# Optimization experiments

Measured on AMD Instinct MI355X. Metric: run time of the kernel, lower is better.

## Reference

```python
import jax, jax.numpy as jnp
import numpy as np
import itertools

DIM = 384; KEY_DIM = 32; NH = 8; RES = 7; N = RES * RES
D = 4 * KEY_DIM; DH = D * NH; NHKD = KEY_DIM * NH; HID = 4 * DIM
B = 512
SCALE = KEY_DIM ** -0.5

def ste_round(x):
    return x + jax.lax.stop_gradient(jnp.round(x) - x)

def ste_floor(x):
    return x + jax.lax.stop_gradient(jnp.floor(x) - x)

def quant_act(x, bits=8):
    # dynamic per-tensor symmetric fake-quant (QuantAct)
    qmax = 2.0 ** (bits - 1) - 1
    s = jnp.maximum(jnp.max(jnp.abs(x)) / qmax, 1e-8)
    return jnp.clip(ste_round(x / s), -qmax, qmax) * s, s

def quant_w(w, bits=8):
    # per-output-channel symmetric weight fake-quant
    qmax = 2.0 ** (bits - 1) - 1
    red = tuple(range(1, w.ndim))
    s = jnp.maximum(jnp.max(jnp.abs(w), axis=red, keepdims=True) / qmax, 1e-8)
    return jnp.clip(ste_round(w / s), -qmax, qmax) * s

def conv(x, w, b, stride=1, pad=0, groups=1):
    # QuantBNConv2d with BN folded into (w, b)
    y = jax.lax.conv_general_dilated(
        x, quant_w(w), (stride, stride), [(pad, pad), (pad, pad)],
        dimension_numbers=('NCHW', 'OIHW', 'NCHW'), feature_group_count=groups)
    return y + b[None, :, None, None]

def head_mix(attn, w, b):
    # talking-heads 1x1 QuantConv2d over the head axis
    return jnp.einsum('oi,bixy->boxy', quant_w(w)[:, :, 0, 0], attn) + b[None, :, None, None]

def int_softmax(x, sf, out_bit=16):
    # I-BERT style integer softmax (2nd-order poly approx of exp) over last axis
    n = 30
    c0 = 0.35815147
    x_int = x / sf
    x_int = x_int - jnp.max(x_int, axis=-1, keepdims=True)
    x0_int = jnp.floor(-0.6931 / sf)  # ln(2) in integer domain
    x_int = jnp.maximum(x_int, n * x0_int)
    q = ste_floor(x_int / x0_int)
    r = x_int - x0_int * q
    b_int = jnp.floor((0.96963238 / c0) / sf)
    c_int = jnp.floor((1.0 / c0) / (sf * sf))
    z = (r + b_int) * r + c_int
    exp_int = jnp.clip(ste_floor(z * jnp.exp2(n - q)), 0.0, None)
    exp, exp_sf = quant_act(exp_int * (c0 * sf * sf / 2.0 ** n), 16)
    exp_int = exp / exp_sf
    factor = ste_floor(2.0 ** 32 / jnp.sum(exp_int, axis=-1, keepdims=True))
    exp_int = ste_floor(exp_int * factor / 2.0 ** (32 - out_bit))
    sf_out = 1.0 / 2.0 ** out_bit
    return exp_int * sf_out, sf_out

def _forward(x, act_sf, wq, bq, wk, bk, wv, bv, wvl, bvl, attn_biases,
             wth1, bth1, wth2, bth2, wproj, bproj,
             wfc1, bfc1, wmid, bmid, wfc2, bfc2, ls1, ls2, bias_idxs):
    Bn = x.shape[0]
    # --- token mixer (Q_Attention4D, stride=None) ---
    q, _ = quant_act(conv(x, wq, bq))
    q = q.reshape(Bn, NH, KEY_DIM, N).transpose(0, 1, 3, 2)   # (B,H,N,kd)
    k, _ = quant_act(conv(x, wk, bk))
    k = k.reshape(Bn, NH, KEY_DIM, N)                          # (B,H,kd,N)
    vf, _ = quant_act(conv(x, wv, bv))
    vl, _ = quant_act(conv(vf, wvl, bvl, pad=1, groups=DH))    # depthwise 3x3 local branch
    v = vf.reshape(Bn, NH, D, N).transpose(0, 1, 3, 2)         # (B,H,N,d)
    attn = jnp.einsum('bhnk,bhkm->bhnm', q, k) * SCALE
    attn = attn + attn_biases[:, bias_idxs]                    # (H,N,N) relative position bias
    attn, _ = quant_act(attn, 8)                               # quant_pre_th1
    attn = head_mix(attn, wth1, bth1)                          # talking_head1
    attn, a_sf = quant_act(attn, 8)                            # quant_attn
    attn, a_sf = int_softmax(attn, a_sf, 16)
    attn = head_mix(attn, wth2, bth2)                          # talking_head2
    attn, _ = quant_act(attn, 8)                               # quant_postsm
    out = jnp.einsum('bhnm,bhmd->bhnd', attn, v)
    out = out.transpose(0, 1, 3, 2).reshape(Bn, DH, RES, RES) + vl
    out, _ = quant_act(out)                                    # quant_av_res
    out = jax.nn.relu(out)                                     # proj_act
    out, _ = quant_act(out)                                    # proj_in_quant
    out = conv(out, wproj, bproj)
    out, _ = quant_act(out)                                    # proj_quant
    x1, _ = quant_act(x + ls1[None] * out)                     # residual 1 + quant_res1
    # --- Q_Mlp (mid_conv=True, ReLU) ---
    h = jax.nn.relu(conv(x1, wfc1, bfc1))
    h, _ = quant_act(h)
    h = jax.nn.relu(conv(h, wmid, bmid, pad=1, groups=HID))
    h, _ = quant_act(h)
    h = conv(h, wfc2, bfc2)
    h, _ = quant_act(h)
    out2, out_sf = quant_act(x1 + ls2[None] * h)               # residual 2 + quant_res2
    return out2, out_sf

def setup_inputs():
    key = jax.random.key(0)
    ks = jax.random.split(key, 16)
    rn = lambda k, shp: (0.02 * jax.random.normal(k, shp)).astype(jnp.float32)
    z = lambda n: jnp.zeros((n,), jnp.float32)
    # rebuild attention_bias_idxs exactly as in __init__
    pts = list(itertools.product(range(RES), range(RES)))
    offs, idxs = {}, []
    for p1 in pts:
        for p2 in pts:
            o = (abs(p1[0] - p2[0]), abs(p1[1] - p2[1]))
            if o not in offs:
                offs[o] = len(offs)
            idxs.append(offs[o])
    bias_idxs = jnp.asarray(np.array(idxs, dtype=np.int32).reshape(N, N))
    return dict(
        x=jax.random.normal(ks[0], (B, DIM, RES, RES), jnp.float32),
        act_sf=jnp.ones((1,), jnp.float32),
        wq=rn(ks[1], (NHKD, DIM, 1, 1)), bq=z(NHKD),
        wk=rn(ks[2], (NHKD, DIM, 1, 1)), bk=z(NHKD),
        wv=rn(ks[3], (DH, DIM, 1, 1)), bv=z(DH),
        wvl=rn(ks[4], (DH, 1, 3, 3)), bvl=z(DH),
        attn_biases=rn(ks[5], (NH, len(offs))),
        wth1=rn(ks[6], (NH, NH, 1, 1)), bth1=z(NH),
        wth2=rn(ks[7], (NH, NH, 1, 1)), bth2=z(NH),
        wproj=rn(ks[8], (DIM, DH, 1, 1)), bproj=z(DIM),
        wfc1=rn(ks[9], (HID, DIM, 1, 1)), bfc1=z(HID),
        wmid=rn(ks[10], (HID, 1, 3, 3)), bmid=z(HID),
        wfc2=rn(ks[11], (DIM, HID, 1, 1)), bfc2=z(DIM),
        ls1=1e-5 * jnp.ones((DIM, 1, 1), jnp.float32),
        ls2=1e-5 * jnp.ones((DIM, 1, 1), jnp.float32),
        bias_idxs=bias_idxs)

def reference(x, act_sf, wq, bq, wk, bk, wv, bv, wvl, bvl, attn_biases,
              wth1, bth1, wth2, bth2, wproj, bproj,
              wfc1, bfc1, wmid, bmid, wfc2, bfc2, ls1, ls2, bias_idxs):
    return _forward(x, act_sf, wq, bq, wk, bk, wv, bv, wvl, bvl, attn_biases,
                    wth1, bth1, wth2, bth2, wproj, bproj,
                    wfc1, bfc1, wmid, bmid, wfc2, bfc2, ls1, ls2, bias_idxs)
```

## Files before the change

### kernel.cpp

```cpp
#include <hip/hip_runtime.h>

typedef unsigned short u16;
typedef unsigned int u32;
typedef float f32x4 __attribute__((ext_vector_type(4)));
typedef short bf16x8 __attribute__((ext_vector_type(8)));
typedef short s16x4 __attribute__((ext_vector_type(4)));


__device__ __forceinline__ u16 f2bf(float f){
  u32 x = __float_as_uint(f);
  x += 0x7fffu + ((x >> 16) & 1u);
  return (u16)(x >> 16);
}
__device__ __forceinline__ float bf2f(u16 u){ return __uint_as_float(((u32)u) << 16); }
__device__ __forceinline__ float qsc(float m, float qmax){ return fmaxf(m / qmax, 1e-8f); }
__device__ __forceinline__ float fq(float x, float s){
  return fminf(fmaxf(rintf(x / s), -127.f), 127.f) * s;
}
__device__ __forceinline__ float fqi(float x, float s, float inv){
  return fminf(fmaxf(rintf(x * inv), -127.f), 127.f) * s;
}
__device__ __forceinline__ float rdmx(const float* mx, int reg){
  float m = mx[reg];
  #pragma unroll
  for (int s = 1; s < 16; ++s) m = fmaxf(m, mx[s*64 + reg]);
  return m;
}
__device__ __forceinline__ void blockMaxTo(float* mx, int reg, float v){
  __shared__ float red[8];
  #pragma unroll
  for (int o = 32; o > 0; o >>= 1) v = fmaxf(v, __shfl_xor(v, o, 64));
  const int wid = threadIdx.x >> 6;
  const int nw = (int)(blockDim.x + 63) >> 6;
  __syncthreads();
  if ((threadIdx.x & 63) == 0) red[wid] = v;
  __syncthreads();
  if (threadIdx.x == 0){
    float m = red[0];
    for (int i = 1; i < nw; ++i) m = fmaxf(m, red[i]);
    const int slot = (blockIdx.x + blockIdx.y*4) & 15;
    atomicMax((int*)&mx[slot*64 + reg], __float_as_int(m));
  }
}
__device__ __forceinline__ void blockMax2To(float* mx, int r0i, float v0, int r1i, float v1){
  __shared__ float r0[8], r1[8];
  #pragma unroll
  for (int o = 32; o > 0; o >>= 1){
    v0 = fmaxf(v0, __shfl_xor(v0, o, 64));
    v1 = fmaxf(v1, __shfl_xor(v1, o, 64));
  }
  const int wid = threadIdx.x >> 6;
  const int nw = (int)(blockDim.x + 63) >> 6;
  __syncthreads();
  if ((threadIdx.x & 63) == 0){ r0[wid] = v0; r1[wid] = v1; }
  __syncthreads();
  if (threadIdx.x == 0){
    float m0 = r0[0], m1 = r1[0];
    for (int i = 1; i < nw; ++i){ m0 = fmaxf(m0, r0[i]); m1 = fmaxf(m1, r1[i]); }
    const int slot = (blockIdx.x + blockIdx.y*4) & 15;
    atomicMax((int*)&mx[slot*64 + r0i], __float_as_int(m0));
    atomicMax((int*)&mx[slot*64 + r1i], __float_as_int(m1));
  }
}

__device__ __forceinline__ void gload16(const void* g, void* l){
  __builtin_amdgcn_global_load_lds((const __attribute__((address_space(1))) u32*)g,
                                   (__attribute__((address_space(3))) u32*)l, 16, 0, 0);
}

__global__ void zeromx(float* mx){
  for (int j = threadIdx.x; j < 1024; j += 256) mx[j] = 0.f;
}

__global__ __launch_bounds__(128) void wquant(
    const float* wq, const float* wk, const float* wv, const float* wproj,
    const float* wfc1, const float* wfc2, const float* wvl, const float* wmid,
    const float* wth1, const float* wth2,
    const float* bq, const float* bk, const float* bv,
    const float* ab, const int* idxs,
    u16* wqkv_b, u16* wproj_b, u16* wfc1_b, u16* wfc2_b,
    float* wvl_q, float* wmid_q, float* wth1_q, float* wth2_q, float* biasqkv,
    float* biasx)
{
  const int tid = threadIdx.x;
  const int bid = blockIdx.x;
  if (bid == 6416){
    for (int j = tid; j < 1536; j += 128){
      float v = (j < 256) ? bq[j] : ((j < 512) ? bk[j - 256] : bv[j - 512]);
      biasqkv[j] = v;
    }
    return;
  }
  if (bid >= 6417){
    const int h = bid - 6417;
    for (int j = tid; j < 2401; j += 128)
      biasx[h*2401 + j] = ab[h*49 + idxs[j]];
    return;
  }
  const int rows[10] = {256,256,1024,384,1536,384,1024,1536,8,8};
  int seg = 0, r = bid;
  while (r >= rows[seg]) { r -= rows[seg]; ++seg; }
  int len = 0;
  const float* src = nullptr; u16* db = nullptr; float* df = nullptr;
  switch (seg){
    case 0: len = 384;  src = wq    + r*384;  db = wqkv_b + r*384;        break;
    case 1: len = 384;  src = wk    + r*384;  db = wqkv_b + (256+r)*384;  break;
    case 2: len = 384;  src = wv    + r*384;  db = wqkv_b + (512+r)*384;  break;
    case 3: len = 1024; src = wproj + r*1024; db = wproj_b + r*1024;      break;
    case 4: len = 384;  src = wfc1  + r*384;  db = wfc1_b + r*384;        break;
    case 5: len = 1536; src = wfc2  + r*1536; db = wfc2_b + r*1536;       break;
    case 6: len = 9;    src = wvl   + r*9;    df = wvl_q + r*9;           break;
    case 7: len = 9;    src = wmid  + r*9;    df = wmid_q + r*9;          break;
    case 8: len = 8;    src = wth1  + r*8;    df = wth1_q + r*8;          break;
    default: len = 8;   src = wth2  + r*8;    df = wth2_q + r*8;          break;
  }
  float lm = 0.f;
  for (int j = tid; j < len; j += 128) lm = fmaxf(lm, fabsf(src[j]));
  __shared__ float red[128];
  red[tid] = lm; __syncthreads();
  for (int s = 64; s > 0; s >>= 1){
    if (tid < s) red[tid] = fmaxf(red[tid], red[tid + s]);
    __syncthreads();
  }
  float s = fmaxf(red[0] / 127.f, 1e-8f);
  for (int j = tid; j < len; j += 128){
    float v = fminf(fmaxf(rintf(src[j] / s), -127.f), 127.f) * s;
    if (db) db[j] = f2bf(v); else df[j] = v;
  }
}

__global__ __launch_bounds__(256) void xpose(const float* __restrict__ x, u16* __restrict__ xT){
  const int b = blockIdx.x;
  __shared__ u16 xb[18816];
  const int tid = threadIdx.x;
  for (int jj = tid; jj < 4704; jj += 256){
    const float4 v = *(const float4*)&x[(size_t)b*18816 + jj*4];
    xb[jj*4+0] = f2bf(v.x); xb[jj*4+1] = f2bf(v.y);
    xb[jj*4+2] = f2bf(v.z); xb[jj*4+3] = f2bf(v.w);
  }
  __syncthreads();
  for (int jj = tid; jj < 4704; jj += 256){
    int j = jj*4, p = j / 384, c = j - p*384;
    s16x4 o;
    #pragma unroll
    for (int u = 0; u < 4; ++u) o[u] = (short)xb[(c+u)*49 + p];
    *(s16x4*)&xT[(size_t)b*18816 + j] = o;
  }
}

__global__ __launch_bounds__(256) void gemm_bt(
    const u16* __restrict__ A, const u16* __restrict__ Bt,
    const float* __restrict__ bias, u16* __restrict__ C,
    float* __restrict__ mx, int N, int K, int epi, int region, int aquant)
{
  const int nx = gridDim.x;
  const int nwg = nx * gridDim.y;
  const int orig = blockIdx.x + nx * blockIdx.y;
  const int q8 = nwg >> 3, r8 = nwg & 7;
  const int xcd = orig & 7;
  const int lid = ((xcd < r8) ? xcd*(q8+1) : r8*(q8+1) + (xcd - r8)*q8) + (orig >> 3);
  const int n0 = (lid % nx) * 128;
  const int m0 = (lid / nx) * 128;
  __shared__ __align__(16) u16 As[128*64];
  __shared__ __align__(16) u16 Bs[128*64];
  const int tid = threadIdx.x;
  const int lane = tid & 63, wid = tid >> 6;
  const int wr = wid >> 1, wc = wid & 1;
  float qa_s0 = 1.f, qa_i0 = 1.f, qa_s1 = 1.f, qa_i1 = 1.f;
  if (aquant == 1){
    qa_s0 = qsc(rdmx(mx,7), 127.f); qa_i0 = 1.f/qa_s0;
    float posq = fq(rdmx(mx,8), qa_s0);
    qa_s1 = fmaxf(posq / 127.f, 1e-8f); qa_i1 = 1.f/qa_s1;
  } else if (aquant == 2){
    qa_s0 = qsc(rdmx(mx,12), 127.f); qa_i0 = 1.f/qa_s0;
  }
  f32x4 acc[4][4] = {};
  const int nsteps = K >> 6;
  for (int s = 0; s < nsteps; ++s){
    const int k0 = s << 6;
    #pragma unroll
    for (int j = 0; j < 4; ++j){
      int boff = j*4096 + tid*16;
      int row = boff >> 7;
      int ce  = (((boff & 127) ^ ((row & 7) << 4)) >> 1);
      if (aquant == 0){
        gload16(A + (size_t)(m0 + row)*K + k0 + ce, (char*)As + boff);
      } else {
        uint4 va = *(const uint4*)(A + (size_t)(m0 + row)*K + k0 + ce);
        u16* e = (u16*)&va;
        #pragma unroll
        for (int u = 0; u < 8; ++u){
          float f = bf2f(e[u]);
          if (aquant == 1){
            f = fmaxf(fqi(f, qa_s0, qa_i0), 0.f);
            f = fqi(f, qa_s1, qa_i1);
          } else {
            f = fqi(f, qa_s0, qa_i0);
          }
          e[u] = f2bf(f);
        }
        *(uint4*)((char*)As + boff) = va;
      }
      gload16(Bt + (size_t)(n0 + row)*K + k0 + ce, (char*)Bs + boff);
    }
    __syncthreads();
    #pragma unroll
    for (int kk = 0; kk < 2; ++kk){
      bf16x8 af[4], bfr[4];
      #pragma unroll
      for (int i = 0; i < 4; ++i){
        int ar = wr*64 + i*16 + (lane & 15);
        int aidx = (ar*64 + kk*32 + (lane >> 4)*8) ^ ((ar & 7) << 3);
        af[i]  = *(const bf16x8*)&As[aidx];
        int br = wc*64 + i*16 + (lane & 15);
        int bidx = (br*64 + kk*32 + (lane >> 4)*8) ^ ((br & 7) << 3);
        bfr[i] = *(const bf16x8*)&Bs[bidx];
      }
      #pragma unroll
      for (int i = 0; i < 4; ++i){
        #pragma unroll
        for (int j = 0; j < 4; ++j){
          acc[i][j] = __builtin_amdgcn_mfma_f32_16x16x32_bf16(af[i], bfr[j], acc[i][j], 0, 0, 0);
        }
      }
    }
    __syncthreads();
  }
  float lm = 0.f;
  #pragma unroll
  for (int i = 0; i < 4; ++i){
    int rbase = m0 + wr*64 + i*16 + ((lane >> 4) << 2);
    #pragma unroll
    for (int j = 0; j < 4; ++j){
      int col = n0 + wc*64 + j*16 + (lane & 15);
      float bv = bias[col];
      #pragma unroll
      for (int q = 0; q < 4; ++q){
        float v = acc[i][j][q] + bv;
        if (epi == 2) v = fmaxf(v, 0.f);
        C[(size_t)(rbase + q)*N + col] = f2bf(v);
        lm = fmaxf(lm, (epi == 2) ? v : fabsf(v));
      }
    }
  }
  int reg = region;
  if (epi == 1) reg = (n0 < 256) ? 0 : ((n0 < 512) ? 1 : 2);
  blockMaxTo(mx, reg, lm);
}

__global__ __launch_bounds__(256) void attn_qk(
    const u16* __restrict__ qkv, const float* __restrict__ biasx,
    const float* __restrict__ wv9, const float* __restrict__ bvl,
    u16* __restrict__ S, u16* __restrict__ vlb, float* __restrict__ mx)
{
  const int h = blockIdx.x;
  __shared__ __align__(16) float xin[6272];
  __shared__ __align__(16) u16 Qb[64*40];
  __shared__ __align__(16) u16 Kb[64*40];
  const float sq = qsc(rdmx(mx,0), 127.f), sk = qsc(rdmx(mx,1), 127.f), sv = qsc(rdmx(mx,2), 127.f);
  const float iq = 1.f/sq, ik = 1.f/sk, iv = 1.f/sv;
  const int tid = threadIdx.x;
  const int lane = tid & 63, wid = tid >> 6;
  const int c = tid & 127, half = tid >> 7;
  float w9[9];
  #pragma unroll
  for (int t = 0; t < 9; ++t) w9[t] = wv9[h*1152 + c*9 + t];
  const float bb = bvl[h*128 + c];
  const float sscale = (sq * sk) * 0.17677669529663687f;
  const float* bx = biasx + h*2401;
  const int col = wid*16 + (lane & 15);
  float lm = 0.f, lmV = 0.f;
  for (int bb4 = 0; bb4 < 4; ++bb4){
    const int b = blockIdx.y*4 + bb4;
    __syncthreads();
    for (int j = tid; j < 196; j += 256){
      int n = j >> 2, d0 = (j & 3)*8;
      size_t base = (size_t)(b*49 + n)*1536;
      const bf16x8 qv = *(const bf16x8*)&qkv[base + h*32 + d0];
      const bf16x8 kv = *(const bf16x8*)&qkv[base + 256 + h*32 + d0];
      bf16x8 qo, ko;
      #pragma unroll
      for (int u = 0; u < 8; ++u){
        qo[u] = (short)f2bf(fminf(fmaxf(rintf(bf2f((u16)qv[u]) * iq), -127.f), 127.f));
        ko[u] = (short)f2bf(fminf(fmaxf(rintf(bf2f((u16)kv[u]) * ik), -127.f), 127.f));
      }
      *(bf16x8*)&Qb[n*40 + d0] = qo;
      *(bf16x8*)&Kb[n*40 + d0] = ko;
    }
    for (int j = tid; j < 784; j += 256){
      int p = j >> 4, dg = j & 15;
      const bf16x8 vv = *(const bf16x8*)&qkv[(size_t)(b*49 + p)*1536 + 512 + h*128 + dg*8];
      #pragma unroll
      for (int u = 0; u < 8; ++u)
        xin[p*128 + dg*8 + u] = fqi(bf2f((u16)vv[u]), sv, iv);
    }
    __syncthreads();
    {
      const int p0 = half*25, p1 = half ? 49 : 25;
      for (int p = p0; p < p1; ++p){
        const int py = p / 7, px = p - py*7;
        float acc = bb;
        #pragma unroll
        for (int dy = 0; dy < 3; ++dy){
          const int yy = py + dy - 1;
          if (yy < 0 || yy > 6) continue;
          #pragma unroll
          for (int dx = 0; dx < 3; ++dx){
            const int xx = px + dx - 1;
            if (xx < 0 || xx > 6) continue;
            acc += xin[(yy*7 + xx)*128 + c] * w9[dy*3 + dx];
          }
        }
        lmV = fmaxf(lmV, fabsf(acc));
        vlb[(size_t)(b*49 + p)*1024 + h*128 + c] = f2bf(acc);
      }
    }
    f32x4 acc[4] = {};
    {
      const bf16x8 bfr = *(const bf16x8*)&Kb[(wid*16 + (lane & 15))*40 + (lane >> 4)*8];
      #pragma unroll
      for (int i = 0; i < 4; ++i){
        const bf16x8 af = *(const bf16x8*)&Qb[(i*16 + (lane & 15))*40 + (lane >> 4)*8];
        acc[i] = __builtin_amdgcn_mfma_f32_16x16x32_bf16(af, bfr, acc[i], 0, 0, 0);
      }
    }
    if (col < 49){
      const size_t so = ((size_t)b*8 + h)*2401;
      #pragma unroll
      for (int i = 0; i < 4; ++i){
        #pragma unroll
        for (int q = 0; q < 4; ++q){
          const int row = i*16 + ((lane >> 4) << 2) + q;
          if (row < 49){
            float v = acc[i][q] * sscale + bx[row*49 + col];
            S[so + row*49 + col] = f2bf(v);
            lm = fmaxf(lm, fabsf(v));
          }
        }
      }
    }
  }
  blockMax2To(mx, 4, lm, 3, lmV);
}

__global__ __launch_bounds__(256) void th1k(
    const u16* S, const float* w1, const float* b1, u16* T, float* mx)
{
  const int b = blockIdx.y;
  const int j = blockIdx.x*256 + threadIdx.x;
  __shared__ float wsh[64];
  __shared__ float bsh[8];
  if (threadIdx.x < 64) wsh[threadIdx.x] = w1[threadIdx.x];
  if (threadIdx.x < 8)  bsh[threadIdx.x] = b1[threadIdx.x];
  __syncthreads();
  float lm = 0.f;
  if (j < 2401){
    const float s1 = qsc(rdmx(mx,4), 127.f);
    const float i1 = 1.f/s1;
    float a[8];
    #pragma unroll
    for (int h = 0; h < 8; ++h) a[h] = fqi(bf2f(S[((size_t)b*8 + h)*2401 + j]), s1, i1);
    float o8[8];
    #pragma unroll
    for (int o = 0; o < 8; ++o){
      float t = bsh[o];
      #pragma unroll
      for (int h = 0; h < 8; ++h) t += wsh[o*8 + h] * a[h];
      o8[o] = t;
      lm = fmaxf(lm, fabsf(t));
    }
    #pragma unroll
    for (int o = 0; o < 8; ++o) T[((size_t)b*8 + o)*2401 + j] = f2bf(o8[o]);
  }
  blockMaxTo(mx, 5, lm);
}

__global__ __launch_bounds__(256) void smth2(
    const u16* T, const float* w2, const float* b2, u16* U, float* mx)
{
  const int b = blockIdx.x;
  __shared__ u16 P[19208];
  __shared__ float wsh[64];
  __shared__ float bsh[8];
  const float sa = qsc(rdmx(mx,5), 127.f), ia = 1.f/sa;
  const int tid = threadIdx.x;
  if (tid < 64) wsh[tid] = w2[tid];
  if (tid < 8)  bsh[tid] = b2[tid];
  for (int j = tid; j < 19208; j += 256){
    float k = fminf(fmaxf(rintf(bf2f(T[(size_t)b*19208 + j]) * ia), -127.f), 127.f);
    P[j] = f2bf(k);
  }
  __syncthreads();
  const float x0 = floorf(-0.6931f / sa);
  const float ix0 = 1.f / x0;
  const float bi = floorf((0.96963238f / 0.35815147f) / sa);
  const float ci = floorf((1.0f / 0.35815147f) / (sa * sa));
  const float Kc = ((0.35815147f * sa) * sa) * (1.f/1073741824.f);
  const float maxv = (ci * 1073741824.f) * Kc;
  const float se = fmaxf(maxv / 32767.f, 1e-8f);
  const float ise = 1.f / se;
  const float clampLo = 30.f * x0;
  for (int r = tid; r < 392; r += 256){
    u16* pr = &P[r*49];
    float rmax = -1e30f;
    for (int m = 0; m < 49; ++m) rmax = fmaxf(rmax, bf2f(pr[m]));
    float rsum = 0.f;
    for (int m = 0; m < 49; ++m){
      float xi = bf2f(pr[m]) - rmax;
      xi = fmaxf(xi, clampLo);
      float qd = floorf(xi * ix0);
      float rr = xi - x0*qd;
      float z = (rr + bi)*rr + ci;
      float ei = fmaxf(floorf(z * exp2f(30.f - qd)), 0.f);
      float e2 = fminf(fmaxf(rintf((ei * Kc) * ise), -32767.f), 32767.f);
      u16 eb = f2bf(e2);
      pr[m] = eb;
      rsum += bf2f(eb);
    }
    const float factor = floorf(4294967296.f / rsum);
    for (int m = 0; m < 49; ++m){
      float p = floorf((bf2f(pr[m]) * factor) * (1.f/65536.f)) * (1.f/65536.f);
      pr[m] = f2bf(p);
    }
  }
  __syncthreads();
  float lm = 0.f;
  for (int j = tid; j < 19208; j += 256){
    int o = j / 2401, rem = j - o*2401;
    float t = bsh[o];
    #pragma unroll
    for (int h = 0; h < 8; ++h) t += wsh[o*8 + h] * bf2f(P[h*2401 + rem]);
    U[(size_t)b*19208 + j] = f2bf(t);
    lm = fmaxf(lm, fabsf(t));
  }
  blockMaxTo(mx, 6, lm);
}

__global__ __launch_bounds__(256) void attn_v(
    const u16* __restrict__ qkv, const u16* __restrict__ U,
    u16* __restrict__ av, float* __restrict__ mx)
{
  const int h = blockIdx.x, b = blockIdx.y;
  __shared__ __align__(16) u16 Pb[64*68];
  __shared__ __align__(16) u16 Vt[128*66];
  const float s3 = qsc(rdmx(mx,6), 127.f), sv = qsc(rdmx(mx,2), 127.f), svl = qsc(rdmx(mx,3), 127.f);
  const float i3 = 1.f/s3, iv = 1.f/sv, il = 1.f/svl;
  const float s3sv = s3 * sv;
  const int tid = threadIdx.x;
  const int lane = tid & 63, wid = tid >> 6;
  const int col0 = wid * 32;
  const int ca = col0 + (lane & 15), cb = ca + 16;
  u16 vlrA[16], vlrB[16];
  {
    const size_t vbase = (size_t)(b*49)*1024 + h*128;
    #pragma unroll
    for (int i = 0; i < 4; ++i){
      #pragma unroll
      for (int q = 0; q < 4; ++q){
        const int row = i*16 + ((lane >> 4) << 2) + q;
        const int rr = (row < 49) ? row : 48;
        vlrA[i*4+q] = av[vbase + (size_t)rr*1024 + ca];
        vlrB[i*4+q] = av[vbase + (size_t)rr*1024 + cb];
      }
    }
  }
  for (int j = tid; j < 64*19; j += 256){ int n = j/19, m = 49 + (j - n*19); Pb[n*68 + m] = 0; }
  for (int j = tid; j < 128*17; j += 256){ int d = j/17, m = 49 + (j - d*17); Vt[d*66 + m] = 0; }
  for (int j = tid; j < 2401; j += 256){
    int n = j / 49, m = j - n*49;
    float k = fminf(fmaxf(rintf(bf2f(U[((size_t)b*8 + h)*2401 + j]) * i3), -127.f), 127.f);
    Pb[n*68 + m] = f2bf(k);
  }
  {
    const int dp = lane * 2, mc = wid;
    const int mend = (mc == 3) ? 49 : (mc*13 + 13);
    const size_t base = (size_t)(b*49)*1536 + 512 + h*128 + dp;
    for (int m = mc*13; m < mend; ++m){
      u32 two = *(const u32*)&qkv[base + (size_t)m*1536];
      float k0 = fminf(fmaxf(rintf(bf2f((u16)(two & 0xffffu)) * iv), -127.f), 127.f);
      float k1 = fminf(fmaxf(rintf(bf2f((u16)(two >> 16)) * iv), -127.f), 127.f);
      Vt[dp*66 + m]       = f2bf(k0);
      Vt[(dp + 1)*66 + m] = f2bf(k1);
    }
  }
  __syncthreads();
  f32x4 acc[4][2] = {};
  #pragma unroll
  for (int kk = 0; kk < 2; ++kk){
    bf16x8 af[4], bfr[2];
    #pragma unroll
    for (int i = 0; i < 4; ++i)
      af[i] = *(const bf16x8*)&Pb[(i*16 + (lane & 15))*68 + kk*32 + (lane >> 4)*8];
    #pragma unroll
    for (int j = 0; j < 2; ++j)
      bfr[j] = *(const bf16x8*)&Vt[(col0 + j*16 + (lane & 15))*66 + kk*32 + (lane >> 4)*8];
    #pragma unroll
    for (int i = 0; i < 4; ++i)
      #pragma unroll
      for (int j = 0; j < 2; ++j)
        acc[i][j] = __builtin_amdgcn_mfma_f32_16x16x32_bf16(af[i], bfr[j], acc[i][j], 0, 0, 0);
  }
  float lm = 0.f, lmp = 0.f;
  #pragma unroll
  for (int i = 0; i < 4; ++i){
    #pragma unroll
    for (int q = 0; q < 4; ++q){
      const int row = i*16 + ((lane >> 4) << 2) + q;
      if (row < 49){
        const size_t base = (size_t)(b*49 + row)*1024 + h*128;
        const float vlA = fqi(bf2f(vlrA[i*4+q]), svl, il);
        const float vlB = fqi(bf2f(vlrB[i*4+q]), svl, il);
        const float vA = acc[i][0][q] * s3sv + vlA;
        const float vB = acc[i][1][q] * s3sv + vlB;
        av[base + ca] = f2bf(vA);
        av[base + cb] = f2bf(vB);
        lm = fmaxf(lm, fmaxf(fabsf(vA), fabsf(vB)));
        lmp = fmaxf(lmp, fmaxf(vA, vB));
      }
    }
  }
  blockMax2To(mx, 7, lm, 8, lmp);
}

__global__ __launch_bounds__(256) void res1max(
    const float* __restrict__ x, const u16* __restrict__ praw,
    const float* __restrict__ ls1, float* __restrict__ y1, float* __restrict__ mx)
{
  const int b = blockIdx.x;
  __shared__ float xs[18816];
  __shared__ float lss[384];
  const float sp = qsc(rdmx(mx,9), 127.f);
  const float ip = 1.f / sp;
  const int tid = threadIdx.x;
  for (int jj = tid; jj < 4704; jj += 256)
    *(float4*)&xs[jj*4] = *(const float4*)&x[(size_t)b*18816 + jj*4];
  for (int j = tid; j < 384; j += 256) lss[j] = ls1[j];
  __syncthreads();
  float lm = 0.f;
  for (int jj = tid; jj < 4704; jj += 256){
    int j = jj*4, p = j / 384, c = j - p*384;
    s16x4 pv = *(const s16x4*)&praw[(size_t)b*18816 + j];
    float4 yv;
    #pragma unroll
    for (int u = 0; u < 4; ++u){
      float y = xs[(c+u)*49 + p] + lss[c+u] * fqi(bf2f((u16)pv[u]), sp, ip);
      ((float*)&yv)[u] = y;
      lm = fmaxf(lm, fabsf(y));
    }
    *(float4*)&y1[(size_t)b*18816 + j] = yv;
  }
  blockMaxTo(mx, 10, lm);
}

__global__ void qx1(const float* __restrict__ y1, float* __restrict__ x1f, u16* __restrict__ x1b,
                    const float* __restrict__ mx){
  const float s = qsc(rdmx(mx,10), 127.f);
  const size_t n4 = (size_t)9633792/4;
  for (size_t i = (size_t)blockIdx.x*blockDim.x + threadIdx.x; i < n4; i += (size_t)gridDim.x*blockDim.x){
    float4 v = *(const float4*)(y1 + i*4);
    float4 o; s16x4 ob;
    #pragma unroll
    for (int u = 0; u < 4; ++u){
      float q = fq(((const float*)&v)[u], s);
      ((float*)&o)[u] = q;
      ob[u] = (short)f2bf(q);
    }
    *(float4*)(x1f + i*4) = o;
    *(s16x4*)(x1b + i*4) = ob;
  }
}

__global__ __launch_bounds__(128) void dw_mid(
    const u16* h1, const float* wm9, const float* bmid, u16* m1, float* mx)
{
  const int cc = blockIdx.x, b = blockIdx.y;
  __shared__ float xin[49*132];
  const float sh = qsc(rdmx(mx,11), 127.f);
  const float ih = 1.f / sh;
  const int tid = threadIdx.x;
  for (int j = tid; j < 784; j += 128){
    int p = j >> 4, dg = j & 15;
    const bf16x8 vv = *(const bf16x8*)&h1[(size_t)(b*49 + p)*1536 + cc*128 + dg*8];
    #pragma unroll
    for (int u = 0; u < 8; ++u)
      xin[p*132 + dg*8 + u] = fqi(bf2f((u16)vv[u]), sh, ih);
  }
  __syncthreads();
  const int c = tid;
  float w9[9];
  #pragma unroll
  for (int i = 0; i < 9; ++i) w9[i] = wm9[(cc*128 + c)*9 + i];
  const float bb = bmid[cc*128 + c];
  float col[49];
  #pragma unroll
  for (int p = 0; p < 49; ++p) col[p] = xin[p*132 + c];
  float lm = 0.f;
  #pragma unroll
  for (int p = 0; p < 49; ++p){
    const int py = p / 7, px = p % 7;
    float acc = bb;
    #pragma unroll
    for (int dy = 0; dy < 3; ++dy){
      const int yy = py + dy - 1;
      if (yy < 0 || yy > 6) continue;
      #pragma unroll
      for (int dx = 0; dx < 3; ++dx){
        const int xx = px + dx - 1;
        if (xx < 0 || xx > 6) continue;
        acc += col[yy*7 + xx] * w9[dy*3 + dx];
      }
    }
    acc = fmaxf(acc, 0.f);
    m1[(size_t)(b*49 + p)*1536 + cc*128 + c] = f2bf(acc);
    lm = fmaxf(lm, acc);
  }
  blockMaxTo(mx, 12, lm);
}

__global__ __launch_bounds__(256) void res2max(
    const float* __restrict__ x1f, const u16* __restrict__ f2,
    const float* __restrict__ ls2, float* __restrict__ y2, float* __restrict__ mx)
{
  const float s = qsc(rdmx(mx,13), 127.f);
  const float is = 1.f / s;
  float lm = 0.f;
  const size_t n4 = (size_t)9633792/4;
  for (size_t i = (size_t)blockIdx.x*blockDim.x + threadIdx.x; i < n4; i += (size_t)gridDim.x*blockDim.x){
    int c0 = (int)((i*4) % 384);
    float4 xv = *(const float4*)(x1f + i*4);
    s16x4 fv = *(const s16x4*)(f2 + i*4);
    float4 yv;
    #pragma unroll
    for (int u = 0; u < 4; ++u){
      float y = ((const float*)&xv)[u] + ls2[c0+u] * fqi(bf2f((u16)fv[u]), s, is);
      ((float*)&yv)[u] = y;
      lm = fmaxf(lm, fabsf(y));
    }
    *(float4*)(y2 + i*4) = yv;
  }
  blockMaxTo(mx, 14, lm);
}

__global__ __launch_bounds__(256) void finalout(
    const float* __restrict__ y2, float* __restrict__ out, const float* __restrict__ mx)
{
  const int b = blockIdx.x;
  __shared__ float os[18816];
  const float s = qsc(rdmx(mx,14), 127.f);
  const int tid = threadIdx.x;
  for (int jj = tid; jj < 4704; jj += 256){
    int j = jj*4, p = j / 384, c = j - p*384;
    float4 yv = *(const float4*)&y2[(size_t)b*18816 + j];
    #pragma unroll
    for (int u = 0; u < 4; ++u)
      os[(c+u)*49 + p] = fq(((const float*)&yv)[u], s);
  }
  __syncthreads();
  for (int jj = tid; jj < 4704; jj += 256)
    *(float4*)&out[(size_t)b*18816 + jj*4] = *(const float4*)&os[jj*4];
  if (b == 0 && tid == 0) out[9633792] = s;
}

extern "C" void kernel_launch(void* const* d_in, const int* in_sizes, int n_in,
                              void* d_out, int out_size, void* d_ws, size_t ws_size,
                              hipStream_t stream)
{
  (void)in_sizes; (void)n_in; (void)out_size; (void)ws_size;
  const float* x    = (const float*)d_in[0];
  const float* wq   = (const float*)d_in[2];
  const float* bq   = (const float*)d_in[3];
  const float* wk   = (const float*)d_in[4];
  const float* bk   = (const float*)d_in[5];
  const float* wv   = (const float*)d_in[6];
  const float* bv   = (const float*)d_in[7];
  const float* wvl  = (const float*)d_in[8];
  const float* bvl  = (const float*)d_in[9];
  const float* ab   = (const float*)d_in[10];
  const float* wth1 = (const float*)d_in[11];
  const float* bth1 = (const float*)d_in[12];
  const float* wth2 = (const float*)d_in[13];
  const float* bth2 = (const float*)d_in[14];
  const float* wproj= (const float*)d_in[15];
  const float* bproj= (const float*)d_in[16];
  const float* wfc1 = (const float*)d_in[17];
  const float* bfc1 = (const float*)d_in[18];
  const float* wmid = (const float*)d_in[19];
  const float* bmid = (const float*)d_in[20];
  const float* wfc2 = (const float*)d_in[21];
  const float* bfc2 = (const float*)d_in[22];
  const float* ls1  = (const float*)d_in[23];
  const float* ls2  = (const float*)d_in[24];
  const int*   idxs = (const int*)d_in[25];
  float* out = (float*)d_out;

  char* w = (char*)d_ws;
  float* biasqkv = (float*)(w + 256);
  u16* wqkv_b    = (u16*)(w + 6400);
  u16* wproj_b   = (u16*)(w + 1186048);
  u16* wfc1_b    = (u16*)(w + 1972480);
  u16* wfc2_b    = (u16*)(w + 3152128);
  float* wvl_q   = (float*)(w + 4331776);
  float* wmid_q  = (float*)(w + 4368640);
  float* wth1_q  = (float*)(w + 4423936);
  float* wth2_q  = (float*)(w + 4424192);
  u16* xT    = (u16*)(w + 4424448);
  u16* praw  = xT;
  u16* x1b   = xT;
  u16* f2raw = xT;
  u16* qkv = (u16*)(w + 23692032);
  u16* h1  = qkv;
  u16* avb = (u16*)(w + 100762368);
  u16* Sb   = (u16*)(w + 152142592);
  float* y1 = (float*)(w + 152142592);
  float* y2 = y1;
  float* biasx = (float*)(w + 190677760);
  float* mx = (float*)(w + 190754816);
  float* x1f = out;

  zeromx<<<1, 256, 0, stream>>>(mx);
  wquant<<<6425, 128, 0, stream>>>(wq, wk, wv, wproj, wfc1, wfc2, wvl, wmid, wth1, wth2,
                                   bq, bk, bv, ab, idxs,
                                   wqkv_b, wproj_b, wfc1_b, wfc2_b,
                                   wvl_q, wmid_q, wth1_q, wth2_q, biasqkv, biasx);
  xpose<<<512, 256, 0, stream>>>(x, xT);
  gemm_bt<<<dim3(12, 196), 256, 0, stream>>>(xT, wqkv_b, biasqkv, qkv, mx, 1536, 384, 1, 0, 0);
  attn_qk<<<dim3(8, 128), 256, 0, stream>>>(qkv, biasx, wvl_q, bvl, Sb, avb, mx);
  th1k<<<dim3(10, 512), 256, 0, stream>>>(Sb, wth1_q, bth1, Sb, mx);
  smth2<<<512, 256, 0, stream>>>(Sb, wth2_q, bth2, Sb, mx);
  attn_v<<<dim3(8, 512), 256, 0, stream>>>(qkv, Sb, avb, mx);
  gemm_bt<<<dim3(3, 196), 256, 0, stream>>>(avb, wproj_b, bproj, praw, mx, 384, 1024, 0, 9, 1);
  res1max<<<512, 256, 0, stream>>>(x, praw, ls1, y1, mx);
  qx1<<<2048, 256, 0, stream>>>(y1, x1f, x1b, mx);
  gemm_bt<<<dim3(12, 196), 256, 0, stream>>>(x1b, wfc1_b, bfc1, h1, mx, 1536, 384, 2, 11, 0);
  dw_mid<<<dim3(12, 512), 128, 0, stream>>>(h1, wmid_q, bmid, h1, mx);
  gemm_bt<<<dim3(3, 196), 256, 0, stream>>>(h1, wfc2_b, bfc2, f2raw, mx, 384, 1536, 0, 13, 2);
  res2max<<<2048, 256, 0, stream>>>(x1f, f2raw, ls2, y2, mx);
  finalout<<<512, 256, 0, stream>>>(y2, out, mx);
}
```

Before: 557.2 us.

## Use 256x128 tiles with XCD-aware block remap for QKV and FC1 GEMMs

Adds a gemm_bt2 kernel that computes a 256x128 output tile per block, reusing each B fragment across two A halves. Block IDs are remapped so consecutive tiles land on the same XCD for better L2 locality. It is used for the QKV and FC1 GEMMs (N=1536, K=384) and halves the grid. The kernel is single-buffered with more accumulator registers, which risks lower occupancy and fewer blocks to spread across CUs.

```diff
diff --git a/kernel.cpp b/kernel.cpp
--- a/kernel.cpp
+++ b/kernel.cpp
@@ -240,6 +240,92 @@
         if (epi == 2) v = fmaxf(v, 0.f);
         C[(size_t)(rbase + q)*N + col] = f2bf(v);
         lm = fmaxf(lm, (epi == 2) ? v : fabsf(v));
+      }
+    }
+  }
+  int reg = region;
+  if (epi == 1) reg = (n0 < 256) ? 0 : ((n0 < 512) ? 1 : 2);
+  blockMaxTo(mx, reg, lm);
+}
+
+__global__ __launch_bounds__(256) void gemm_bt2(
+    const u16* __restrict__ A, const u16* __restrict__ Bt,
+    const float* __restrict__ bias, u16* __restrict__ C,
+    float* __restrict__ mx, int N, int K, int epi, int region)
+{
+  const int nx = gridDim.x;
+  const int nwg = nx * gridDim.y;
+  const int orig = blockIdx.x + nx * blockIdx.y;
+  const int q8 = nwg >> 3, r8 = nwg & 7;
+  const int xcd = orig & 7;
+  const int lid = ((xcd < r8) ? xcd*(q8+1) : r8*(q8+1) + (xcd - r8)*q8) + (orig >> 3);
+  const int n0 = (lid % nx) * 128;
+  const int m0 = (lid / nx) * 256;
+  __shared__ __align__(16) u16 As[2][128*64];
+  __shared__ __align__(16) u16 Bs[128*64];
+  const int tid = threadIdx.x;
+  const int lane = tid & 63, wid = tid >> 6;
+  const int wr = wid >> 1, wc = wid & 1;
+  f32x4 acc[2][4][4] = {};
+  const int nsteps = K >> 6;
+  for (int s = 0; s < nsteps; ++s){
+    const int k0 = s << 6;
+    #pragma unroll
+    for (int j = 0; j < 4; ++j){
+      int boff = j*4096 + tid*16;
+      int row = boff >> 7;
+      int ce  = (((boff & 127) ^ ((row & 7) << 4)) >> 1);
+      gload16(A + (size_t)(m0 + row)*K + k0 + ce,        (char*)As[0] + boff);
+      gload16(A + (size_t)(m0 + 128 + row)*K + k0 + ce,  (char*)As[1] + boff);
+      gload16(Bt + (size_t)(n0 + row)*K + k0 + ce,       (char*)Bs + boff);
+    }
+    __syncthreads();
+    #pragma unroll
+    for (int kk = 0; kk < 2; ++kk){
+      bf16x8 bfr[4];
+      #pragma unroll
+      for (int i = 0; i < 4; ++i){
+        int br = wc*64 + i*16 + (lane & 15);
+        int bidx = (br*64 + kk*32 + (lane >> 4)*8) ^ ((br & 7) << 3);
+        bfr[i] = *(const bf16x8*)&Bs[bidx];
+      }
+      #pragma unroll
+      for (int h = 0; h < 2; ++h){
+        bf16x8 af[4];
+        #pragma unroll
+        for (int i = 0; i < 4; ++i){
+          int ar = wr*64 + i*16 + (lane & 15);
+          int aidx = (ar*64 + kk*32 + (lane >> 4)*8) ^ ((ar & 7) << 3);
+          af[i] = *(const bf16x8*)&As[h][aidx];
+        }
+        #pragma unroll
+        for (int i = 0; i < 4; ++i){
+          #pragma unroll
+          for (int j = 0; j < 4; ++j){
+            acc[h][i][j] = __builtin_amdgcn_mfma_f32_16x16x32_bf16(af[i], bfr[j], acc[h][i][j], 0, 0, 0);
+          }
+        }
+      }
+    }
+    __syncthreads();
+  }
+  float lm = 0.f;
+  #pragma unroll
+  for (int h = 0; h < 2; ++h){
+    #pragma unroll
+    for (int i = 0; i < 4; ++i){
+      int rbase = m0 + h*128 + wr*64 + i*16 + ((lane >> 4) << 2);
+      #pragma unroll
+      for (int j = 0; j < 4; ++j){
+        int col = n0 + wc*64 + j*16 + (lane & 15);
+        float bv = bias[col];
+        #pragma unroll
+        for (int q = 0; q < 4; ++q){
+          float v = acc[h][i][j][q] + bv;
+          if (epi == 2) v = fmaxf(v, 0.f);
+          C[(size_t)(rbase + q)*N + col] = f2bf(v);
+          lm = fmaxf(lm, (epi == 2) ? v : fabsf(v));
+        }
       }
     }
   }
@@ -723,7 +809,7 @@
                                    wqkv_b, wproj_b, wfc1_b, wfc2_b,
                                    wvl_q, wmid_q, wth1_q, wth2_q, biasqkv, biasx);
   xpose<<<512, 256, 0, stream>>>(x, xT);
-  gemm_bt<<<dim3(12, 196), 256, 0, stream>>>(xT, wqkv_b, biasqkv, qkv, mx, 1536, 384, 1, 0, 0);
+  gemm_bt2<<<dim3(12, 98), 256, 0, stream>>>(xT, wqkv_b, biasqkv, qkv, mx, 1536, 384, 1, 0);
   attn_qk<<<dim3(8, 128), 256, 0, stream>>>(qkv, biasx, wvl_q, bvl, Sb, avb, mx);
   th1k<<<dim3(10, 512), 256, 0, stream>>>(Sb, wth1_q, bth1, Sb, mx);
   smth2<<<512, 256, 0, stream>>>(Sb, wth2_q, bth2, Sb, mx);
@@ -731,7 +817,7 @@
   gemm_bt<<<dim3(3, 196), 256, 0, stream>>>(avb, wproj_b, bproj, praw, mx, 384, 1024, 0, 9, 1);
   res1max<<<512, 256, 0, stream>>>(x, praw, ls1, y1, mx);
   qx1<<<2048, 256, 0, stream>>>(y1, x1f, x1b, mx);
-  gemm_bt<<<dim3(12, 196), 256, 0, stream>>>(x1b, wfc1_b, bfc1, h1, mx, 1536, 384, 2, 11, 0);
+  gemm_bt2<<<dim3(12, 98), 256, 0, stream>>>(x1b, wfc1_b, bfc1, h1, mx, 1536, 384, 2, 11);
   dw_mid<<<dim3(12, 512), 128, 0, stream>>>(h1, wmid_q, bmid, h1, mx);
   gemm_bt<<<dim3(3, 196), 256, 0, stream>>>(h1, wfc2_b, bfc2, f2raw, mx, 384, 1536, 0, 13, 2);
   res2max<<<2048, 256, 0, stream>>>(x1f, f2raw, ls2, y2, mx);
```

Measured after the change: 607.0 us. +8.9%, slower.
